# Optimization experiments

Measured on AMD Instinct MI355X. Metric: run time of the kernel, lower is better.

Reference implementation:

```python
import jax, jax.numpy as jnp
import numpy as np

# Module config (matches init_kwargs)
C = 256          # in_channels
H = 8            # num_heads
T, L = 32, 16    # partition_size
S = T * L        # tokens per window = 512
B_ = 64          # number of windows
SCALE = H ** (-0.5)  # faithful to source: num_heads**-0.5


def setup_inputs() -> dict:
    key = jax.random.key(0)
    ks = jax.random.split(key, 6)
    x = jax.random.normal(ks[0], (B_, S, C), dtype=jnp.float32)
    # nn.Linear(C, 3C) weights: [out, in], bias: [out]
    qkv_w = jax.random.normal(ks[1], (3 * C, C), dtype=jnp.float32) * (1.0 / np.sqrt(C))
    qkv_b = jnp.zeros((3 * C,), dtype=jnp.float32)
    proj_w = jax.random.normal(ks[2], (C, C), dtype=jnp.float32) * (1.0 / np.sqrt(C))
    proj_b = jnp.zeros((C,), dtype=jnp.float32)
    # relative_position_bias_table for type_2: (2T-1, L, L, H), trunc_normal std=0.02 ~ small normal
    rel_table = jax.random.normal(ks[3], (2 * T - 1, L, L, H), dtype=jnp.float32) * 0.02
    return {"x": x, "qkv_w": qkv_w, "qkv_b": qkv_b,
            "proj_w": proj_w, "proj_b": proj_b, "rel_table": rel_table}


def _relative_position_bias(rel_table):
    # 1D relative index over T temporal positions, values in [0, 2T-2]
    idx = jnp.arange(T)[:, None] - jnp.arange(T)[None, :] + (T - 1)  # [T, T]
    b = rel_table[idx]                        # [T, T, L, L, H]
    b = b.transpose(0, 2, 1, 3, 4)            # [T, L, T, L, H]
    b = b.reshape(S, S, H)                    # [S, S, H]
    return b.transpose(2, 0, 1)[None]         # [1, H, S, S]


def reference(x, qkv_w, qkv_b, proj_w, proj_b, rel_table):
    Bw, Sw, Cw = x.shape
    d = Cw // H
    qkv = x @ qkv_w.T + qkv_b                              # [B_, S, 3C]
    qkv = qkv.reshape(Bw, Sw, 3, H, d).transpose(2, 0, 3, 1, 4)  # [3, B_, H, S, d]
    q, k, v = qkv[0], qkv[1], qkv[2]
    attn = jnp.einsum('bhsd,bhtd->bhst', q * SCALE, k)     # [B_, H, S, S]
    attn = attn + _relative_position_bias(rel_table)
    attn = jax.nn.softmax(attn, axis=-1)
    # attn_drop p=0.0 -> identity
    out = jnp.einsum('bhst,bhtd->bhsd', attn, v)           # [B_, H, S, d]
    out = out.transpose(0, 2, 1, 3).reshape(Bw, Sw, Cw)    # [B_, S, C]
    out = out @ proj_w.T + proj_b
    # proj_drop p=0.0 -> identity
    return out
```

## Files before the change

### kernel.cpp

```cpp
#include <hip/hip_runtime.h>
#include <stdint.h>

#define NB 64
#define NS 512
#define NC 256
#define NH 8
#define ND 32

typedef __attribute__((ext_vector_type(8))) short s8v;
typedef __attribute__((ext_vector_type(8))) unsigned short u8v;
typedef __attribute__((ext_vector_type(4))) float f4v;

#define LOG2E 1.4426950408889634f

static __device__ __forceinline__ uint16_t f2bf(float f) {
    uint32_t u = __builtin_bit_cast(uint32_t, f);
    u += 0x7fffu + ((u >> 16) & 1u);
    return (uint16_t)(u >> 16);
}
static __device__ __forceinline__ float bf2f(uint16_t h) {
    uint32_t u = ((uint32_t)h) << 16;
    return __builtin_bit_cast(float, u);
}
static __device__ __forceinline__ uint32_t cvtpk(float lo, float hi) {
    uint32_t r;
    asm("v_cvt_pk_bf16_f32 %0, %1, %2" : "=v"(r) : "v"(lo), "v"(hi));
    return r;
}

#if __has_builtin(__builtin_amdgcn_permlane32_swap)
static __device__ __forceinline__ void pl32(uint32_t& a, uint32_t& b) {
    auto r = __builtin_amdgcn_permlane32_swap(a, b, false, false);
    a = r[0]; b = r[1];
}
static __device__ __forceinline__ void pl16(uint32_t& a, uint32_t& b) {
    auto r = __builtin_amdgcn_permlane16_swap(a, b, false, false);
    a = r[0]; b = r[1];
}
#else
static __device__ __forceinline__ void pl32(uint32_t& a, uint32_t& b) {
    asm volatile("v_permlane32_swap_b32 %0, %1" : "+v"(a), "+v"(b));
}
static __device__ __forceinline__ void pl16(uint32_t& a, uint32_t& b) {
    asm volatile("v_permlane16_swap_b32 %0, %1" : "+v"(a), "+v"(b));
}
#endif

__global__ __launch_bounds__(256) void setup_kern(const float* __restrict__ rel,
                                                  const float* __restrict__ wq,
                                                  const float* __restrict__ wp,
                                                  uint16_t* __restrict__ rel2,
                                                  uint16_t* __restrict__ wqo,
                                                  uint16_t* __restrict__ wpo) {
    const int bid = blockIdx.x;
    if (bid < 640) {
        int id = bid * 256 + threadIdx.x;
        int h = id / 20480, rem = id % 20480;
        int dt = rem / 320, q = rem % 320;
        int li = q / 20, lj = q % 20;
        float v = (lj < 16 && dt < 63) ? rel[(((dt << 4) + li) * 16 + lj) * 8 + h] * LOG2E : 0.f;
        rel2[id] = f2bf(v);
    } else {
        int i = ((bid - 640) * 256 + threadIdx.x) * 8;
        const float* src; uint16_t* dst; int off;
        if (i < 196608) { src = wq; dst = wqo; off = i; }
        else            { src = wp; dst = wpo; off = i - 196608; }
        f4v a = *(const f4v*)(src + off);
        f4v b = *(const f4v*)(src + off + 4);
        uint4 w;
        w.x = cvtpk(a[0], a[1]); w.y = cvtpk(a[2], a[3]);
        w.z = cvtpk(b[0], b[1]); w.w = cvtpk(b[2], b[3]);
        *(uint4*)(dst + off) = w;
    }
}

__global__ __launch_bounds__(256) void qkv_gemm(const float* __restrict__ X,
                                                const uint16_t* __restrict__ W,
                                                const float* __restrict__ Bv,
                                                uint16_t* __restrict__ Qo,
                                                uint16_t* __restrict__ Ko,
                                                uint16_t* __restrict__ Vo) {
    __shared__ uint16_t As[2][64 * 40];
    __shared__ uint16_t Bs[2][128 * 40];
    const int tid = threadIdx.x;
    const int bn = blockIdx.y * 128;
    const int bm = blockIdx.x * 64;
    const int lane = tid & 63, wv = tid >> 6;
    const int wm = (wv >> 1) * 32, wn = (wv & 1) * 64;
    const int lq = lane & 15, g = lane >> 4;
    const int arow = tid >> 2, acol = (tid & 3) * 8;
    const int srow = tid >> 1, scol = (tid & 1) * 16;

    const float* xs = X + (size_t)(bm + arow) * 256 + acol;
    const uint16_t* wsrc = W + (size_t)(bn + srow) * 256 + scol;

    f4v acc[2][4] = {};
    f4v xr[2][2];
    u8v wr[2][2];

#define LOAD_S(set, kel)                                                    \
    do {                                                                    \
        xr[set][0] = *(const f4v*)(xs + (kel));                             \
        xr[set][1] = *(const f4v*)(xs + (kel) + 4);                         \
        wr[set][0] = *(const u8v*)(wsrc + (kel));                           \
        wr[set][1] = *(const u8v*)(wsrc + (kel) + 8);                       \
    } while (0)

#define STORE_S(buf, set)                                                   \
    do {                                                                    \
        uint4 q0;                                                           \
        q0.x = cvtpk(xr[set][0][0], xr[set][0][1]);                         \
        q0.y = cvtpk(xr[set][0][2], xr[set][0][3]);                         \
        q0.z = cvtpk(xr[set][1][0], xr[set][1][1]);                         \
        q0.w = cvtpk(xr[set][1][2], xr[set][1][3]);                         \
        *(uint4*)(&As[buf][arow * 40 + acol]) = q0;                         \
        *(u8v*)(&Bs[buf][srow * 40 + scol])     = wr[set][0];               \
        *(u8v*)(&Bs[buf][srow * 40 + scol + 8]) = wr[set][1];               \
    } while (0)

    LOAD_S(0, 0);
    LOAD_S(1, 32);
    STORE_S(0, 0);
    __syncthreads();

    #pragma unroll
    for (int ks = 0; ks < 8; ++ks) {
        const int cur = ks & 1;
        if (ks + 2 < 8) LOAD_S(cur, (ks + 2) * 32);
        s8v af[2], bf[4];
        #pragma unroll
        for (int i = 0; i < 2; ++i)
            af[i] = *(const s8v*)(&As[cur][(wm + i * 16 + lq) * 40 + g * 8]);
        #pragma unroll
        for (int i = 0; i < 4; ++i)
            bf[i] = *(const s8v*)(&Bs[cur][(wn + i * 16 + lq) * 40 + g * 8]);
        #pragma unroll
        for (int mt = 0; mt < 2; ++mt)
            #pragma unroll
            for (int nt = 0; nt < 4; ++nt)
                acc[mt][nt] = __builtin_amdgcn_mfma_f32_16x16x32_bf16(af[mt], bf[nt], acc[mt][nt], 0, 0, 0);
        if (ks < 7) STORE_S(cur ^ 1, (ks + 1) & 1);
        __syncthreads();
    }
#undef LOAD_S
#undef STORE_S

    const int gsel = bn >> 8;
    if (gsel == 2) {
        #pragma unroll
        for (int nt = 0; nt < 4; ++nt) {
            const int ng = bn + wn + nt * 16 + lq;
            const float bv = Bv[ng];
            const int c = ng & 255, hh = c >> 5, dd = c & 31;
            f4v u = acc[0][nt], v = acc[1][nt];
            uint32_t A0 = cvtpk(u[0] + bv, u[1] + bv);
            uint32_t A1 = cvtpk(u[2] + bv, u[3] + bv);
            uint32_t B0 = cvtpk(v[0] + bv, v[1] + bv);
            uint32_t B1 = cvtpk(v[2] + bv, v[3] + bv);
            pl32(A0, B0); pl16(A0, B0);
            pl32(A1, B1); pl16(A1, B1);
            uint4 wq; wq.x = A0; wq.y = A1; wq.z = B0; wq.w = B1;
            const int m0 = bm + wm;
            const int b = m0 >> 9;
            const int s0 = (m0 & 511) + g * 8;
            *(uint4*)(Vo + ((size_t)(b * 8 + hh) * 32 + dd) * 512 + s0) = wq;
        }
    } else {
        const float scl = (gsel == 0) ? (0.35355339059327373f * LOG2E) : 1.0f;
        #pragma unroll
        for (int nt = 0; nt < 4; ++nt) {
            const int ng = bn + wn + nt * 16 + lq;
            const float bv = Bv[ng];
            const int c = ng & 255, hh = c >> 5, dd = c & 31;
            #pragma unroll
            for (int mt = 0; mt < 2; ++mt) {
                #pragma unroll
                for (int r = 0; r < 4; ++r) {
                    const int m = bm + wm + mt * 16 + g * 4 + r;
                    const int b = m >> 9, s = m & 511;
                    const uint16_t val = f2bf((acc[mt][nt][r] + bv) * scl);
                    if (gsel == 0) Qo[((size_t)(b * 8 + hh) * 512 + s) * 32 + dd] = val;
                    else           Ko[((size_t)(b * 8 + hh) * 512 + s) * 32 + dd] = val;
                }
            }
        }
    }
}

__global__ __launch_bounds__(512) void attn_kern(const uint16_t* __restrict__ Q,
                                                 const uint16_t* __restrict__ K,
                                                 const uint16_t* __restrict__ V,
                                                 const uint16_t* __restrict__ REL2,
                                                 uint16_t* __restrict__ AO) {
    __shared__ uint16_t Ks[2 * 64 * 40];
    __shared__ uint16_t Vs[2 * 32 * 80];
    __shared__ uint16_t Rel[39 * 320];

    const int p = blockIdx.x;
    const int h  = p & 7;
    const int qq = (p >> 3) & 3;
    const int b  = p >> 5;
    const int tid = threadIdx.x, lane = tid & 63, wv = tid >> 6;
    const int lq = lane & 15, g = lane >> 4;
    const int bh = b * 8 + h;
    const int qw = qq * 128 + wv * 16;

    s8v qf = *(const s8v*)(Q + ((size_t)bh * 512 + qw + lq) * 32 + g * 8);
    const uint16_t* kg = K + (size_t)bh * 16384;
    const uint16_t* vg = V + (size_t)bh * 16384;

    const uint32_t one2 = 0x3F803F80u;
    uint4 onesw; onesw.x = one2; onesw.y = one2; onesw.z = one2; onesw.w = one2;
    const s8v onesv = __builtin_bit_cast(s8v, onesw);

    {
        const uint16_t* rsrc = REL2 + (size_t)h * 20480 + qq * 2560;
        #pragma unroll
        for (int it = 0; it < 4; ++it) {
            int off = it * 4096 + tid * 8;
            if (off < 12480)
                *(u8v*)(Rel + off) = *(const u8v*)(rsrc + off);
        }
    }

    const bool isK = (tid < 256);
    const int t2 = tid & 255;
    const int ktrow = t2 >> 2, ktcol = (t2 & 3) * 8;
    const int vtrow = t2 >> 3, vtcol = (t2 & 7) * 8;
    const uint16_t* gsrc = isK ? (kg + (size_t)ktrow * 32 + ktcol)
                               : (vg + (size_t)vtrow * 512 + vtcol);
    uint16_t* sbase = isK ? Ks : Vs;
    const int loff = isK ? (ktrow * 40 + ktcol) : (vtrow * 80 + vtcol);
    const int gstep = isK ? (64 * 32) : 64;

    f4v o0 = {}, o1 = {}, ol = {};
    float mrow = -3.0e38f;

    u8v sreg = *(const u8v*)(gsrc);
    *(u8v*)(sbase + loff) = sreg;
    __syncthreads();

    for (int tile = 0; tile < 8; ++tile) {
        const int t0 = tile * 64;
        const int cur = tile & 1;
        const uint16_t* ksb = Ks + cur * 2560;
        const uint16_t* vsb = Vs + cur * 2560;

        if (tile < 7) {
            sreg = *(const u8v*)(gsrc + (size_t)(tile + 1) * gstep);
        }

        f4v a0, a1, a2, a3;
        {
            const int tj0 = t0 >> 4;
            const uint16_t* rb = Rel + lq * 20 + g * 4;
            ushort4 z0 = *(const ushort4*)(rb + (wv + 31 - tj0 - 0) * 320);
            ushort4 z1 = *(const ushort4*)(rb + (wv + 31 - tj0 - 1) * 320);
            ushort4 z2 = *(const ushort4*)(rb + (wv + 31 - tj0 - 2) * 320);
            ushort4 z3 = *(const ushort4*)(rb + (wv + 31 - tj0 - 3) * 320);
            a0[0]=bf2f(z0.x); a0[1]=bf2f(z0.y); a0[2]=bf2f(z0.z); a0[3]=bf2f(z0.w);
            a1[0]=bf2f(z1.x); a1[1]=bf2f(z1.y); a1[2]=bf2f(z1.z); a1[3]=bf2f(z1.w);
            a2[0]=bf2f(z2.x); a2[1]=bf2f(z2.y); a2[2]=bf2f(z2.z); a2[3]=bf2f(z2.w);
            a3[0]=bf2f(z3.x); a3[1]=bf2f(z3.y); a3[2]=bf2f(z3.z); a3[3]=bf2f(z3.w);
        }
        a0 = __builtin_amdgcn_mfma_f32_16x16x32_bf16(*(const s8v*)(ksb + ( 0 + lq) * 40 + g * 8), qf, a0, 0, 0, 0);
        a1 = __builtin_amdgcn_mfma_f32_16x16x32_bf16(*(const s8v*)(ksb + (16 + lq) * 40 + g * 8), qf, a1, 0, 0, 0);
        a2 = __builtin_amdgcn_mfma_f32_16x16x32_bf16(*(const s8v*)(ksb + (32 + lq) * 40 + g * 8), qf, a2, 0, 0, 0);
        a3 = __builtin_amdgcn_mfma_f32_16x16x32_bf16(*(const s8v*)(ksb + (48 + lq) * 40 + g * 8), qf, a3, 0, 0, 0);

        float p01 = fmaxf(fmaxf(a0[0], a0[1]), fmaxf(a0[2], a0[3]));
        float p23 = fmaxf(fmaxf(a1[0], a1[1]), fmaxf(a1[2], a1[3]));
        float p45 = fmaxf(fmaxf(a2[0], a2[1]), fmaxf(a2[2], a2[3]));
        float p67 = fmaxf(fmaxf(a3[0], a3[1]), fmaxf(a3[2], a3[3]));
        float pmax = fmaxf(fmaxf(p01, p23), fmaxf(p45, p67));
        pmax = fmaxf(pmax, __shfl_xor(pmax, 16));
        pmax = fmaxf(pmax, __shfl_xor(pmax, 32));

        if (!__all(pmax - mrow <= 8.0f)) {
            float mnew = fmaxf(mrow, pmax);
            float scale = __builtin_amdgcn_exp2f(mrow - mnew);
            float s0 = __shfl(scale, g * 4 + 0);
            float s1 = __shfl(scale, g * 4 + 1);
            float s2 = __shfl(scale, g * 4 + 2);
            float s3 = __shfl(scale, g * 4 + 3);
            o0[0] *= s0; o0[1] *= s1; o0[2] *= s2; o0[3] *= s3;
            o1[0] *= s0; o1[1] *= s1; o1[2] *= s2; o1[3] *= s3;
            ol[0] *= s0; ol[1] *= s1; ol[2] *= s2; ol[3] *= s3;
            mrow = mnew;
        }

        #pragma unroll
        for (int r = 0; r < 4; ++r) {
            a0[r] = __builtin_amdgcn_exp2f(a0[r] - mrow);
            a1[r] = __builtin_amdgcn_exp2f(a1[r] - mrow);
            a2[r] = __builtin_amdgcn_exp2f(a2[r] - mrow);
            a3[r] = __builtin_amdgcn_exp2f(a3[r] - mrow);
        }

        {
            uint32_t A0 = cvtpk(a0[0], a0[1]);
            uint32_t A1 = cvtpk(a0[2], a0[3]);
            uint32_t B0 = cvtpk(a1[0], a1[1]);
            uint32_t B1 = cvtpk(a1[2], a1[3]);
            pl32(A0, B0); pl16(A0, B0);
            pl32(A1, B1); pl16(A1, B1);
            uint4 wq; wq.x = A0; wq.y = A1; wq.z = B0; wq.w = B1;
            s8v pf = __builtin_bit_cast(s8v, wq);
            s8v vf0 = *(const s8v*)(vsb + lq * 80 + g * 8);
            s8v vf2 = *(const s8v*)(vsb + (lq + 16) * 80 + g * 8);
            o0 = __builtin_amdgcn_mfma_f32_16x16x32_bf16(pf, vf0, o0, 0, 0, 0);
            o1 = __builtin_amdgcn_mfma_f32_16x16x32_bf16(pf, vf2, o1, 0, 0, 0);
            ol = __builtin_amdgcn_mfma_f32_16x16x32_bf16(pf, onesv, ol, 0, 0, 0);
        }
        {
            uint32_t A0 = cvtpk(a2[0], a2[1]);
            uint32_t A1 = cvtpk(a2[2], a2[3]);
            uint32_t B0 = cvtpk(a3[0], a3[1]);
            uint32_t B1 = cvtpk(a3[2], a3[3]);
            pl32(A0, B0); pl16(A0, B0);
            pl32(A1, B1); pl16(A1, B1);
            uint4 wq; wq.x = A0; wq.y = A1; wq.z = B0; wq.w = B1;
            s8v pf = __builtin_bit_cast(s8v, wq);
            s8v vf1 = *(const s8v*)(vsb + lq * 80 + 32 + g * 8);
            s8v vf3 = *(const s8v*)(vsb + (lq + 16) * 80 + 32 + g * 8);
            o0 = __builtin_amdgcn_mfma_f32_16x16x32_bf16(pf, vf1, o0, 0, 0, 0);
            o1 = __builtin_amdgcn_mfma_f32_16x16x32_bf16(pf, vf3, o1, 0, 0, 0);
            ol = __builtin_amdgcn_mfma_f32_16x16x32_bf16(pf, onesv, ol, 0, 0, 0);
        }

        if (tile < 7) {
            *(u8v*)(sbase + (cur ^ 1) * 2560 + loff) = sreg;
        }
        __syncthreads();
    }

    #pragma unroll
    for (int r = 0; r < 4; ++r) {
        const float iv = 1.0f / ol[r];
        const int srow = b * 512 + qw + g * 4 + r;
        uint16_t* dst = AO + (size_t)srow * 256 + h * 32 + lq;
        dst[0]  = f2bf(o0[r] * iv);
        dst[16] = f2bf(o1[r] * iv);
    }
}

__global__ __launch_bounds__(256) void proj_gemm(const uint16_t* __restrict__ A,
                                                 const uint16_t* __restrict__ W,
                                                 const float* __restrict__ Bv,
                                                 float* __restrict__ Out) {
    __shared__ uint16_t As[2][128 * 40];
    __shared__ uint16_t Bs[2][128 * 40];
    const int tid = threadIdx.x;
    const int bn = blockIdx.y * 128;
    const int bm = blockIdx.x * 128;
    const int lane = tid & 63, wv = tid >> 6;
    const int wm = (wv >> 1) * 64, wn = (wv & 1) * 64;
    const int lq = lane & 15, g = lane >> 4;
    const int srow = tid >> 1;
    const int scol = (tid & 1) * 16;

    const uint16_t* as = A + (size_t)(bm + srow) * 256 + scol;
    const uint16_t* wsrc = W + (size_t)(bn + srow) * 256 + scol;

    f4v acc[4][4] = {};
    u8v ar[2][2], wr[2][2];

#define LOAD_P(set, kel)                                                    \
    do {                                                                    \
        ar[set][0] = *(const u8v*)(as + (kel));                             \
        ar[set][1] = *(const u8v*)(as + (kel) + 8);                         \
        wr[set][0] = *(const u8v*)(wsrc + (kel));                           \
        wr[set][1] = *(const u8v*)(wsrc + (kel) + 8);                       \
    } while (0)

#define STORE_P(buf, set)                                                   \
    do {                                                                    \
        *(u8v*)(&As[buf][srow * 40 + scol])     = ar[set][0];               \
        *(u8v*)(&As[buf][srow * 40 + scol + 8]) = ar[set][1];               \
        *(u8v*)(&Bs[buf][srow * 40 + scol])     = wr[set][0];               \
        *(u8v*)(&Bs[buf][srow * 40 + scol + 8]) = wr[set][1];               \
    } while (0)

    LOAD_P(0, 0);
    LOAD_P(1, 32);
    STORE_P(0, 0);
    __syncthreads();

    #pragma unroll
    for (int ks = 0; ks < 8; ++ks) {
        const int cur = ks & 1;
        if (ks + 2 < 8) LOAD_P(cur, (ks + 2) * 32);
        s8v af[4], bf[4];
        #pragma unroll
        for (int i = 0; i < 4; ++i) {
            af[i] = *(const s8v*)(&As[cur][(wm + i * 16 + lq) * 40 + g * 8]);
            bf[i] = *(const s8v*)(&Bs[cur][(wn + i * 16 + lq) * 40 + g * 8]);
        }
        #pragma unroll
        for (int mt = 0; mt < 4; ++mt)
            #pragma unroll
            for (int nt = 0; nt < 4; ++nt)
                acc[mt][nt] = __builtin_amdgcn_mfma_f32_16x16x32_bf16(af[mt], bf[nt], acc[mt][nt], 0, 0, 0);
        if (ks < 7) STORE_P(cur ^ 1, (ks + 1) & 1);
        __syncthreads();
    }
#undef LOAD_P
#undef STORE_P

    #pragma unroll
    for (int nt = 0; nt < 4; ++nt) {
        const int n = bn + wn + nt * 16 + lq;
        const float bv = Bv[n];
        #pragma unroll
        for (int mt = 0; mt < 4; ++mt) {
            #pragma unroll
            for (int r = 0; r < 4; ++r) {
                const int mm = bm + wm + mt * 16 + g * 4 + r;
                Out[(size_t)mm * 256 + n] = acc[mt][nt][r] + bv;
            }
        }
    }
}

extern "C" void kernel_launch(void* const* d_in, const int* in_sizes, int n_in,
                              void* d_out, int out_size, void* d_ws, size_t ws_size,
                              hipStream_t stream) {
    const float* x      = (const float*)d_in[0];
    const float* qkv_w  = (const float*)d_in[1];
    const float* qkv_b  = (const float*)d_in[2];
    const float* proj_w = (const float*)d_in[3];
    const float* proj_b = (const float*)d_in[4];
    const float* rel    = (const float*)d_in[5];
    float* out = (float*)d_out;

    uint16_t* ws = (uint16_t*)d_ws;
    const size_t QE = (size_t)NB * NH * NS * ND;
    uint16_t* Qb   = ws;
    uint16_t* Kb   = Qb + QE;
    uint16_t* Vb   = Kb + QE;
    uint16_t* Rb   = Vb + QE;
    uint16_t* REL2 = Rb + QE;
    uint16_t* Wqb  = REL2 + 163840;
    uint16_t* Wpb  = Wqb + 196608;

    setup_kern<<<768, 256, 0, stream>>>(rel, qkv_w, proj_w, REL2, Wqb, Wpb);
    qkv_gemm<<<dim3(512, 6), 256, 0, stream>>>(x, Wqb, qkv_b, Qb, Kb, Vb);
    attn_kern<<<2048, 512, 0, stream>>>(Qb, Kb, Vb, REL2, Rb);
    proj_gemm<<<dim3(256, 2), 256, 0, stream>>>(Rb, Wpb, proj_b, out);
}
```

Baseline: 98.18 us.

## Load QKV GEMM operands directly from global into MFMA fragments, drop LDS staging

The QKV projection GEMM stops staging X and W tiles through double-buffered shared memory. Each wave now loads its own MFMA fragments straight from global memory, converting X to bf16 in registers, with no __syncthreads. This removes LDS traffic and barriers, but the two waves sharing a row or column block now each fetch the same data from global/L2 and the loads are less coalesced.

```diff
diff --git a/kernel.cpp b/kernel.cpp
--- a/kernel.cpp
+++ b/kernel.cpp
@@ -80,70 +80,49 @@
                                                 uint16_t* __restrict__ Qo,
                                                 uint16_t* __restrict__ Ko,
                                                 uint16_t* __restrict__ Vo) {
-    __shared__ uint16_t As[2][64 * 40];
-    __shared__ uint16_t Bs[2][128 * 40];
     const int tid = threadIdx.x;
     const int bn = blockIdx.y * 128;
     const int bm = blockIdx.x * 64;
     const int lane = tid & 63, wv = tid >> 6;
     const int wm = (wv >> 1) * 32, wn = (wv & 1) * 64;
     const int lq = lane & 15, g = lane >> 4;
-    const int arow = tid >> 2, acol = (tid & 3) * 8;
-    const int srow = tid >> 1, scol = (tid & 1) * 16;
-
-    const float* xs = X + (size_t)(bm + arow) * 256 + acol;
-    const uint16_t* wsrc = W + (size_t)(bn + srow) * 256 + scol;
+
+    const float* xb0 = X + (size_t)(bm + wm + lq) * 256 + g * 8;
+    const float* xb1 = xb0 + 16 * 256;
+    const uint16_t* wb = W + (size_t)(bn + wn + lq) * 256 + g * 8;
 
     f4v acc[2][4] = {};
-    f4v xr[2][2];
-    u8v wr[2][2];
-
-#define LOAD_S(set, kel)                                                    \
-    do {                                                                    \
-        xr[set][0] = *(const f4v*)(xs + (kel));                             \
-        xr[set][1] = *(const f4v*)(xs + (kel) + 4);                         \
-        wr[set][0] = *(const u8v*)(wsrc + (kel));                           \
-        wr[set][1] = *(const u8v*)(wsrc + (kel) + 8);                       \
-    } while (0)
-
-#define STORE_S(buf, set)                                                   \
-    do {                                                                    \
-        uint4 q0;                                                           \
-        q0.x = cvtpk(xr[set][0][0], xr[set][0][1]);                         \
-        q0.y = cvtpk(xr[set][0][2], xr[set][0][3]);                         \
-        q0.z = cvtpk(xr[set][1][0], xr[set][1][1]);                         \
-        q0.w = cvtpk(xr[set][1][2], xr[set][1][3]);                         \
-        *(uint4*)(&As[buf][arow * 40 + acol]) = q0;                         \
-        *(u8v*)(&Bs[buf][srow * 40 + scol])     = wr[set][0];               \
-        *(u8v*)(&Bs[buf][srow * 40 + scol + 8]) = wr[set][1];               \
-    } while (0)
-
-    LOAD_S(0, 0);
-    LOAD_S(1, 32);
-    STORE_S(0, 0);
-    __syncthreads();
 
     #pragma unroll
     for (int ks = 0; ks < 8; ++ks) {
-        const int cur = ks & 1;
-        if (ks + 2 < 8) LOAD_S(cur, (ks + 2) * 32);
-        s8v af[2], bf[4];
-        #pragma unroll
-        for (int i = 0; i < 2; ++i)
-            af[i] = *(const s8v*)(&As[cur][(wm + i * 16 + lq) * 40 + g * 8]);
-        #pragma unroll
-        for (int i = 0; i < 4; ++i)
-            bf[i] = *(const s8v*)(&Bs[cur][(wn + i * 16 + lq) * 40 + g * 8]);
-        #pragma unroll
-        for (int mt = 0; mt < 2; ++mt)
-            #pragma unroll
-            for (int nt = 0; nt < 4; ++nt)
-                acc[mt][nt] = __builtin_amdgcn_mfma_f32_16x16x32_bf16(af[mt], bf[nt], acc[mt][nt], 0, 0, 0);
-        if (ks < 7) STORE_S(cur ^ 1, (ks + 1) & 1);
-        __syncthreads();
-    }
-#undef LOAD_S
-#undef STORE_S
+        const int k0 = ks * 32;
+        s8v af0, af1;
+        {
+            f4v a0 = *(const f4v*)(xb0 + k0);
+            f4v a1 = *(const f4v*)(xb0 + k0 + 4);
+            uint4 q;
+            q.x = cvtpk(a0[0], a0[1]); q.y = cvtpk(a0[2], a0[3]);
+            q.z = cvtpk(a1[0], a1[1]); q.w = cvtpk(a1[2], a1[3]);
+            af0 = __builtin_bit_cast(s8v, q);
+        }
+        {
+            f4v a0 = *(const f4v*)(xb1 + k0);
+            f4v a1 = *(const f4v*)(xb1 + k0 + 4);
+            uint4 q;
+            q.x = cvtpk(a0[0], a0[1]); q.y = cvtpk(a0[2], a0[3]);
+            q.z = cvtpk(a1[0], a1[1]); q.w = cvtpk(a1[2], a1[3]);
+            af1 = __builtin_bit_cast(s8v, q);
+        }
+        s8v bf[4];
+        #pragma unroll
+        for (int nt = 0; nt < 4; ++nt)
+            bf[nt] = *(const s8v*)(wb + (size_t)nt * 16 * 256 + k0);
+        #pragma unroll
+        for (int nt = 0; nt < 4; ++nt) {
+            acc[0][nt] = __builtin_amdgcn_mfma_f32_16x16x32_bf16(af0, bf[nt], acc[0][nt], 0, 0, 0);
+            acc[1][nt] = __builtin_amdgcn_mfma_f32_16x16x32_bf16(af1, bf[nt], acc[1][nt], 0, 0, 0);
+        }
+    }
 
     const int gsel = bn >> 8;
     if (gsel == 2) {
```

Measured after the change: 153.1 us. 56.0% more time.
